# Kernel tuning notes

Hardware: AMD Instinct MI355X
Metric: run time of the kernel (lower is better)

The kernel has to match this reference:

```python
import jax, jax.numpy as jnp
import numpy as np

N, FEAT, PROP, HID, OUT = 8192, 128, 3, 256, 64
IN_SMOOTH = (PROP + 1) * FEAT  # 512
PRELU_INIT = 0.25


def prelu(x, a):
    return jnp.where(x > 0, x, a * x)


def setup_inputs() -> dict:
    key = jax.random.key(0)
    ks = jax.random.split(key, 12)
    s = 0.05
    return {
        "ori_feature": jax.random.normal(ks[0], (N, FEAT), jnp.float32),
        "smoothed_feature": jax.random.normal(ks[1], (N, IN_SMOOTH), jnp.float32),
        "processed_feature": jax.random.normal(ks[2], (N, IN_SMOOTH), jnp.float32),
        "universal_re": jax.random.normal(ks[3], (N, N), jnp.float32),
        # smooth-trans linears
        "Ws1": jax.random.normal(ks[4], (HID, IN_SMOOTH), jnp.float32) * s,
        "bs1": jnp.zeros((HID,), jnp.float32),
        "Ws2": jax.random.normal(ks[5], (OUT, HID), jnp.float32) * s,
        "bs2": jnp.zeros((OUT,), jnp.float32),
        # local-trans linears
        "Wl1": jax.random.normal(ks[6], (HID, FEAT), jnp.float32) * s,
        "bl1": jnp.zeros((HID,), jnp.float32),
        "Wl2": jax.random.normal(ks[7], (OUT, HID), jnp.float32) * s,
        "bl2": jnp.zeros((OUT,), jnp.float32),
        # hete-propagate-layer linears
        "Wh1": jax.random.normal(ks[8], (HID, IN_SMOOTH), jnp.float32) * s,
        "bh1": jnp.zeros((HID,), jnp.float32),
        "Wh2": jax.random.normal(ks[9], (OUT, HID), jnp.float32) * s,
        "bh2": jnp.zeros((OUT,), jnp.float32),
        # PReLU slopes (scalar, one per nn.PReLU())
        "a_model": jnp.float32(PRELU_INIT),
        "a_hete": jnp.float32(PRELU_INIT),
    }


def _getre_scale(emb):
    # emb: [N, OUT]
    es = jax.nn.softmax(emb, axis=1)
    re = es @ es.T                              # [N, N]
    d = jnp.diagonal(re)[:, None]               # [N, 1]
    scaling = d @ d.T                            # [N, N]
    re = re / jnp.maximum(jnp.sqrt(scaling), jnp.float32(1e-9))
    re = re - jnp.diag(jnp.diagonal(re))
    return re


def _forward(ori_feature, smoothed_feature, universal_re,
             Ws1, bs1, Ws2, bs2, Wl1, bl1, Wl2, bl2,
             Wh1, bh1, Wh2, bh2, a_model, a_hete):
    beta = jnp.float32(0.0)  # HetePropagateLayer default beta=0
    # smooth path (dropout is identity in eval)
    h = prelu(smoothed_feature @ Ws1.T + bs1, a_model)
    local_smooth_emb = h @ Ws2.T + bs2
    # local path
    g = prelu(ori_feature @ Wl1.T + bl1, a_model)
    local_ori_emb = g @ Wl2.T + bl2
    # hete propagation on input_prop_feature = smoothed_feature
    f = prelu(smoothed_feature @ Wh1.T + bh1, a_hete)
    feature_emb = f @ Wh2.T + bh2                # [N, OUT]
    re = _getre_scale(feature_emb)               # [N, N]
    lre = beta * universal_re + (1.0 - beta) * re
    m = jnp.mean(lre)
    M = jnp.max(lre)
    pos_diff = M - m                             # pos_min = 0
    shifted = lre - m
    # neg branch: -((shifted - (-m)) / (0 - (-m))) = -((shifted + m) / m)
    lre = jnp.where(shifted > 0, shifted / pos_diff, -((shifted + m) / m))
    # add_diag in source effectively adds identity to its input (bug preserved)
    lre = lre + jnp.eye(N, dtype=lre.dtype)
    pos_signal = prelu(lre, a_hete)
    neg_signal = prelu(-lre, a_hete)
    prop_pos = jax.nn.softmax(pos_signal @ feature_emb, axis=1)
    prop_neg = jax.nn.softmax(neg_signal @ feature_emb, axis=1)
    local_message_propagation = (prop_pos - prop_neg + feature_emb) / 2
    return local_ori_emb, local_smooth_emb, local_message_propagation


def reference(ori_feature, smoothed_feature, processed_feature, universal_re,
              Ws1, bs1, Ws2, bs2, Wl1, bl1, Wl2, bl2,
              Wh1, bh1, Wh2, bh2, a_model, a_hete):
    # processed_feature is unused in the original forward (only .to(device))
    return _forward(ori_feature, smoothed_feature, universal_re,
                    Ws1, bs1, Ws2, bs2, Wl1, bl1, Wl2, bl2,
                    Wh1, bh1, Wh2, bh2, a_model, a_hete)
```

## Files before the change

### kernel.cpp

```cpp
#include <hip/hip_runtime.h>
#include <hip/hip_bf16.h>

#define N 8192

typedef _Float16 half_t;
typedef __attribute__((ext_vector_type(8))) _Float16 half8;
typedef __attribute__((ext_vector_type(4))) float f32x4;
typedef unsigned int uint;
typedef unsigned short ushort;

#define MFMA16(a, b, c) __builtin_amdgcn_mfma_f32_16x16x32_f16(a, b, c, 0, 0, 0)

#define RES_SCALE 2048.0f
#define RES_INV   (1.0f / 2048.0f)

union UH8 { int4 i; half8 h; };
__device__ __forceinline__ half8 ldh(const ushort* p) {
    UH8 t; t.i = *(const int4*)p; return t.h;
}
__device__ __forceinline__ ushort h2u(half_t h) {
    union { half_t f; ushort u; } c; c.f = h; return c.u;
}

__device__ __forceinline__ float wave_max(float v) {
#pragma unroll
    for (int o = 32; o > 0; o >>= 1) v = fmaxf(v, __shfl_xor(v, o, 64));
    return v;
}
__device__ __forceinline__ float wave_sum(float v) {
#pragma unroll
    for (int o = 32; o > 0; o >>= 1) v += __shfl_xor(v, o, 64);
    return v;
}

__global__ __launch_bounds__(256) void gemm_bias_act(
    const float* __restrict__ A, const float* __restrict__ W,
    const float* __restrict__ bias, const float* __restrict__ slope_p,
    float* __restrict__ C, int Nc, int K, int act)
{
    __shared__ float As[16][68];
    __shared__ float Bs[16][68];
    const int tid = threadIdx.x;
    const int tx = tid & 15, ty = tid >> 4;
    const int m0 = blockIdx.x * 64, n0 = blockIdx.y * 64;
    const int lr = tid >> 2, lc4 = (tid & 3) * 4;
    const float* Ap = A + (size_t)(m0 + lr) * K + lc4;
    const float* Wp = W + (size_t)(n0 + lr) * K + lc4;
    float acc[4][4] = {};
    float4 av = *(const float4*)(Ap);
    float4 wv = *(const float4*)(Wp);
    for (int k0 = 0; k0 < K; k0 += 16) {
        __syncthreads();
        As[lc4 + 0][lr] = av.x; As[lc4 + 1][lr] = av.y;
        As[lc4 + 2][lr] = av.z; As[lc4 + 3][lr] = av.w;
        Bs[lc4 + 0][lr] = wv.x; Bs[lc4 + 1][lr] = wv.y;
        Bs[lc4 + 2][lr] = wv.z; Bs[lc4 + 3][lr] = wv.w;
        __syncthreads();
        if (k0 + 16 < K) {
            av = *(const float4*)(Ap + k0 + 16);
            wv = *(const float4*)(Wp + k0 + 16);
        }
#pragma unroll
        for (int k = 0; k < 16; ++k) {
            float a_[4], b_[4];
            float4 t = *(const float4*)&As[k][ty * 4];
            a_[0] = t.x; a_[1] = t.y; a_[2] = t.z; a_[3] = t.w;
            t = *(const float4*)&Bs[k][tx * 4];
            b_[0] = t.x; b_[1] = t.y; b_[2] = t.z; b_[3] = t.w;
#pragma unroll
            for (int i = 0; i < 4; ++i)
#pragma unroll
                for (int j = 0; j < 4; ++j)
                    acc[i][j] += a_[i] * b_[j];
        }
    }
    const float slope = *slope_p;
#pragma unroll
    for (int i = 0; i < 4; ++i) {
        const int row = m0 + ty * 4 + i;
        float4 r;
#pragma unroll
        for (int j = 0; j < 4; ++j) {
            float v = acc[i][j] + bias[n0 + tx * 4 + j];
            if (act) v = v > 0.f ? v : slope * v;
            (&r.x)[j] = v;
        }
        *(float4*)(C + (size_t)row * Nc + n0 + tx * 4) = r;
    }
}

__global__ __launch_bounds__(256) void row_softmax_u(
    const float* __restrict__ E, ushort* __restrict__ uh, ushort* __restrict__ ul,
    float* __restrict__ stats)
{
    const int w = threadIdx.x >> 6, lane = threadIdx.x & 63;
    __shared__ float sacc[4][64];
    __shared__ float tacc[4];
    float s_l = 0.f, t_w = 0.f;
    const int base = blockIdx.x * 16 + w * 4;
    for (int r = 0; r < 4; ++r) {
        const int row = base + r;
        float v = E[(size_t)row * 64 + lane];
        float mx = wave_max(v);
        float e = expf(v - mx);
        float tot = wave_sum(e);
        tot = __shfl(tot, 0, 64);
        float es = e / tot;
        float dd = wave_sum(es * es);
        dd = __shfl(dd, 0, 64);
        float uv = es / sqrtf(dd);
        half_t h = (half_t)uv;
        half_t l = (half_t)((uv - (float)h) * RES_SCALE);
        const size_t idx = (size_t)row * 64 + lane;
        uh[idx] = h2u(h); ul[idx] = h2u(l);
        s_l += uv;
        float uu = wave_sum(uv * uv);
        if (lane == 0) t_w += uu;
    }
    sacc[w][lane] = s_l;
    if (lane == 0) tacc[w] = t_w;
    __syncthreads();
    if (threadIdx.x < 64) {
        float tot = sacc[0][threadIdx.x] + sacc[1][threadIdx.x] +
                    sacc[2][threadIdx.x] + sacc[3][threadIdx.x];
        atomicAdd(&stats[threadIdx.x], tot);
    }
    if (threadIdx.x == 0)
        atomicAdd(&stats[64], tacc[0] + tacc[1] + tacc[2] + tacc[3]);
}

__global__ __launch_bounds__(256) void trans_e(
    const float* __restrict__ E, ushort* __restrict__ Et)
{
    __shared__ ushort T[64][72];
    const int ib = blockIdx.x;
    const int r = threadIdx.x >> 2;
    const int c0 = (threadIdx.x & 3) * 16;
#pragma unroll
    for (int q = 0; q < 4; ++q) {
        float4 v = *(const float4*)(E + (size_t)(ib * 64 + r) * 64 + c0 + q * 4);
#pragma unroll
        for (int t = 0; t < 4; ++t)
            T[c0 + q * 4 + t][r] = h2u((half_t)((&v.x)[t]));
    }
    __syncthreads();
    const int c = threadIdx.x >> 2;
    const int j0 = (threadIdx.x & 3) * 16;
    const size_t go = (size_t)c * N + ib * 64 + j0;
    *(int4*)(Et + go)     = *(const int4*)&T[c][j0];
    *(int4*)(Et + go + 8) = *(const int4*)&T[c][j0 + 8];
}

__global__ __launch_bounds__(64) void pass_max_f16(
    const ushort* __restrict__ uh, const ushort* __restrict__ ul,
    float* __restrict__ maxbuf)
{
    const int bx = blockIdx.x;
    const int by = blockIdx.y;
    const int bid = by * 512 + bx;
    const int i0 = bx * 16;
    const int lane = threadIdx.x;
    const int l16 = lane & 15, lg = lane >> 4;
    if (by * 1024 + 1024 <= i0) {
        if (lane == 0) maxbuf[bid] = 0.f;
        return;
    }
    const size_t ao = (size_t)(i0 + l16) * 64 + lg * 8;
    const half8 Ah0 = ldh(uh + ao), Ah1 = ldh(uh + ao + 32);
    const half8 Al0 = ldh(ul + ao), Al1 = ldh(ul + ao + 32);
    float mx = 0.f;
    for (int jn = 0; jn < 64; ++jn) {
        const int j0 = by * 1024 + jn * 16;
        if (j0 + 16 <= i0) continue;
        const size_t bo = (size_t)(j0 + l16) * 64 + lg * 8;
        half8 Bh0 = ldh(uh + bo), Bh1 = ldh(uh + bo + 32);
        half8 Bl0 = ldh(ul + bo), Bl1 = ldh(ul + bo + 32);
        f32x4 s1 = {0.f, 0.f, 0.f, 0.f};
        f32x4 s2 = {0.f, 0.f, 0.f, 0.f};
        s1 = MFMA16(Ah0, Bh0, s1); s1 = MFMA16(Ah1, Bh1, s1);
        s2 = MFMA16(Ah0, Bl0, s2); s2 = MFMA16(Ah1, Bl1, s2);
        s2 = MFMA16(Al0, Bh0, s2); s2 = MFMA16(Al1, Bh1, s2);
        const bool dt = (j0 == i0);
#pragma unroll
        for (int r = 0; r < 4; ++r) {
            float s = fmaf(s2[r], RES_INV, s1[r]);
            bool dg = dt && (lg * 4 + r == l16);
            mx = dg ? mx : fmaxf(mx, s);
        }
    }
    mx = wave_max(mx);
    if (lane == 0) maxbuf[bid] = mx;
}

__global__ __launch_bounds__(256) void fin_m(
    const float* __restrict__ maxbuf, float* __restrict__ stats)
{
    const int t = threadIdx.x;
    float mx = 0.f;
    for (int i = t; i < 4096; i += 256) mx = fmaxf(mx, maxbuf[i]);
    mx = wave_max(mx);
    __shared__ float red[4];
    __shared__ float ssh;
    if ((t & 63) == 0) red[t >> 6] = mx;
    if (t < 64) {
        float s = stats[t];
        float ss = wave_sum(s * s);
        if (t == 0) ssh = ss;
    }
    __syncthreads();
    if (t == 0) {
        stats[65] = fmaxf(fmaxf(red[0], red[1]), fmaxf(red[2], red[3]));
        stats[66] = (ssh - stats[64]) * (1.0f / 67108864.0f);
    }
}

__global__ __launch_bounds__(256, 4) void pass_prop_f16(
    const ushort* __restrict__ uh, const ushort* __restrict__ ul,
    const ushort* __restrict__ Et, const float* __restrict__ stats,
    const float* __restrict__ ah_p, float* __restrict__ Pp, float* __restrict__ Pn)
{
    __shared__ ushort PNs[4][2][16][68];
    const int w = threadIdx.x >> 6, lane = threadIdx.x & 63;
    const int l16 = lane & 15, lg = lane >> 4;
    const int i0 = blockIdx.x * 16;
    const int js = blockIdx.y;
    const float m = stats[66];
    const float Mx = stats[65];
    const float inv_pd = 1.f / (Mx - m);
    const float c1 = -m * inv_pd;
    const float ninv_m = -1.f / m;
    const float a = *ah_p;
    const size_t ao = (size_t)(i0 + l16) * 64 + lg * 8;
    const half8 Ah0 = ldh(uh + ao), Ah1 = ldh(uh + ao + 32);
    const half8 Al0 = ldh(ul + ao), Al1 = ldh(ul + ao + 32);
    f32x4 accP[4], accN[4];
#pragma unroll
    for (int cs = 0; cs < 4; ++cs) {
        accP[cs] = (f32x4){0.f, 0.f, 0.f, 0.f};
        accN[cs] = (f32x4){0.f, 0.f, 0.f, 0.f};
    }
    ushort (*myP)[68] = PNs[w][0];
    ushort (*myN)[68] = PNs[w][1];
    for (int t = 0; t < 8; ++t) {
        const int j0 = (js * 32 + t * 4 + w) * 64;
#pragma unroll
        for (int jn = 0; jn < 4; ++jn) {
            const size_t bo = (size_t)(j0 + jn * 16 + l16) * 64 + lg * 8;
            half8 Bh0 = ldh(uh + bo), Bh1 = ldh(uh + bo + 32);
            half8 Bl0 = ldh(ul + bo), Bl1 = ldh(ul + bo + 32);
            f32x4 s1 = {0.f, 0.f, 0.f, 0.f};
            f32x4 s2 = {0.f, 0.f, 0.f, 0.f};
            s1 = MFMA16(Ah0, Bh0, s1); s1 = MFMA16(Ah1, Bh1, s1);
            s2 = MFMA16(Ah0, Bl0, s2); s2 = MFMA16(Ah1, Bl1, s2);
            s2 = MFMA16(Al0, Bh0, s2); s2 = MFMA16(Al1, Bh1, s2);
            const bool dt = (j0 + jn * 16 == i0);
#pragma unroll
            for (int r = 0; r < 4; ++r) {
                float s = fmaf(s2[r], RES_INV, s1[r]);
                float l = (s > m) ? fmaf(s, inv_pd, c1) : s * ninv_m;
                if (dt && (lg * 4 + r == l16)) l = 1.0f;
                float q = a * l;
                bool gp = l > 0.f;
                float pos = gp ? l : q;
                float neg = -(gp ? q : l);
                myP[lg * 4 + r][jn * 16 + l16] = h2u((half_t)pos);
                myN[lg * 4 + r][jn * 16 + l16] = h2u((half_t)neg);
            }
        }
#pragma unroll
        for (int kc = 0; kc < 2; ++kc) {
            const ushort* pr = &myP[l16][kc * 32 + lg * 8];
            const ushort* nr = &myN[l16][kc * 32 + lg * 8];
            UH8 tp, tn;
            *(int2*)&tp.i       = *(const int2*)pr;
            *(((int2*)&tp.i)+1) = *(const int2*)(pr + 4);
            *(int2*)&tn.i       = *(const int2*)nr;
            *(((int2*)&tn.i)+1) = *(const int2*)(nr + 4);
            const int ecol = j0 + kc * 32 + lg * 8;
#pragma unroll
            for (int cs = 0; cs < 4; ++cs) {
                const size_t eo = (size_t)(cs * 16 + l16) * N + ecol;
                half8 Ef = ldh(Et + eo);
                accP[cs] = MFMA16(tp.h, Ef, accP[cs]);
                accN[cs] = MFMA16(tn.h, Ef, accN[cs]);
            }
        }
    }
    __syncthreads();
    float* scr = (float*)&PNs[0][0][0][0];
    if (w >= 2) {
        float* base = scr + (size_t)(w - 2) * 2048;
#pragma unroll
        for (int cs = 0; cs < 4; ++cs)
#pragma unroll
            for (int r = 0; r < 4; ++r) {
                const int idx = (lg * 4 + r) * 64 + cs * 16 + l16;
                base[idx]        = accP[cs][r];
                base[idx + 1024] = accN[cs][r];
            }
    }
    __syncthreads();
    if (w < 2) {
        const float* src = scr + (size_t)w * 2048;
#pragma unroll
        for (int cs = 0; cs < 4; ++cs)
#pragma unroll
            for (int r = 0; r < 4; ++r) {
                const int idx = (lg * 4 + r) * 64 + cs * 16 + l16;
                accP[cs][r] += src[idx];
                accN[cs][r] += src[idx + 1024];
            }
    }
    __syncthreads();
    if (w == 1) {
#pragma unroll
        for (int cs = 0; cs < 4; ++cs)
#pragma unroll
            for (int r = 0; r < 4; ++r) {
                const int idx = (lg * 4 + r) * 64 + cs * 16 + l16;
                scr[idx]        = accP[cs][r];
                scr[idx + 1024] = accN[cs][r];
            }
    }
    __syncthreads();
    if (w == 0) {
#pragma unroll
        for (int cs = 0; cs < 4; ++cs)
#pragma unroll
            for (int r = 0; r < 4; ++r) {
                const int idx = (lg * 4 + r) * 64 + cs * 16 + l16;
                const size_t off = ((size_t)js * N + i0 + lg * 4 + r) * 64 + cs * 16 + l16;
                Pp[off] = accP[cs][r] + scr[idx];
                Pn[off] = accN[cs][r] + scr[idx + 1024];
            }
    }
}

__global__ __launch_bounds__(256) void fin_msg(
    const float* __restrict__ Pp, const float* __restrict__ Pn,
    const float* __restrict__ E, float* __restrict__ outm)
{
    const int w = threadIdx.x >> 6, lane = threadIdx.x & 63;
    const int row = blockIdx.x * 4 + w;
    float lp = 0.f, ln = 0.f;
#pragma unroll
    for (int js = 0; js < 4; ++js) {
        lp += Pp[((size_t)js * N + row) * 64 + lane];
        ln += Pn[((size_t)js * N + row) * 64 + lane];
    }
    float mp = wave_max(lp);
    float ep = expf(lp - mp);
    float tp = wave_sum(ep); tp = __shfl(tp, 0, 64);
    float sp = ep / tp;
    float mn = wave_max(ln);
    float en = expf(ln - mn);
    float tn = wave_sum(en); tn = __shfl(tn, 0, 64);
    float sn = en / tn;
    outm[(size_t)row * 64 + lane] = (sp - sn + E[(size_t)row * 64 + lane]) * 0.5f;
}

__global__ void init_stats(float* stats)
{
    if (threadIdx.x < 128) stats[threadIdx.x] = 0.f;
}

extern "C" void kernel_launch(void* const* d_in, const int* in_sizes, int n_in,
                              void* d_out, int out_size, void* d_ws, size_t ws_size,
                              hipStream_t stream)
{
    const float* ori = (const float*)d_in[0];
    const float* smo = (const float*)d_in[1];
    const float* Ws1 = (const float*)d_in[4];
    const float* bs1 = (const float*)d_in[5];
    const float* Ws2 = (const float*)d_in[6];
    const float* bs2 = (const float*)d_in[7];
    const float* Wl1 = (const float*)d_in[8];
    const float* bl1 = (const float*)d_in[9];
    const float* Wl2 = (const float*)d_in[10];
    const float* bl2 = (const float*)d_in[11];
    const float* Wh1 = (const float*)d_in[12];
    const float* bh1 = (const float*)d_in[13];
    const float* Wh2 = (const float*)d_in[14];
    const float* bh2 = (const float*)d_in[15];
    const float* am  = (const float*)d_in[16];
    const float* ah  = (const float*)d_in[17];

    float* out_ori = (float*)d_out;
    float* out_smo = out_ori + (size_t)N * 64;
    float* out_msg = out_smo + (size_t)N * 64;

    char* p = (char*)d_ws;
    float* h      = (float*)p;  p += (size_t)N * 256 * 4;
    float* E      = (float*)p;  p += (size_t)N * 64 * 4;
    float* Pp     = (float*)p;  p += (size_t)4 * N * 64 * 4;
    float* Pn     = (float*)p;  p += (size_t)4 * N * 64 * 4;
    ushort* uh    = (ushort*)p; p += (size_t)N * 64 * 2;
    ushort* ul    = (ushort*)p; p += (size_t)N * 64 * 2;
    ushort* Et    = (ushort*)p; p += (size_t)N * 64 * 2;
    float* maxbuf = (float*)p;  p += 4096 * 4;
    float* stats  = (float*)p;

    const dim3 b(256);
    init_stats<<<1, 128, 0, stream>>>(stats);

    gemm_bias_act<<<dim3(128, 4), b, 0, stream>>>(smo, Ws1, bs1, am, h, 256, 512, 1);
    gemm_bias_act<<<dim3(128, 1), b, 0, stream>>>(h, Ws2, bs2, am, out_smo, 64, 256, 0);
    gemm_bias_act<<<dim3(128, 4), b, 0, stream>>>(ori, Wl1, bl1, am, h, 256, 128, 1);
    gemm_bias_act<<<dim3(128, 1), b, 0, stream>>>(h, Wl2, bl2, am, out_ori, 64, 256, 0);
    gemm_bias_act<<<dim3(128, 4), b, 0, stream>>>(smo, Wh1, bh1, ah, h, 256, 512, 1);
    gemm_bias_act<<<dim3(128, 1), b, 0, stream>>>(h, Wh2, bh2, ah, E, 64, 256, 0);

    row_softmax_u<<<512, b, 0, stream>>>(E, uh, ul, stats);
    trans_e<<<128, b, 0, stream>>>(E, Et);
    pass_max_f16<<<dim3(512, 8), dim3(64), 0, stream>>>(uh, ul, maxbuf);
    fin_m<<<1, 256, 0, stream>>>(maxbuf, stats);
    pass_prop_f16<<<dim3(512, 4), b, 0, stream>>>(uh, ul, Et, stats, ah, Pp, Pn);
    fin_msg<<<2048, b, 0, stream>>>(Pp, Pn, E, out_msg);
}
```

Before: 744.2 us.

## Use split-f16 MFMA GEMMs for linears and regroup max pass into 4-wave blocks

Replaces the scalar FP32 tiled GEMM for the six linear layers with an MFMA kernel that splits inputs and weights into high and low f16 parts and accumulates three products, emulating FP32 accuracy on matrix cores. New split kernels convert inputs and weights each call, and the hidden activations are stored as split f16 pairs. The max pass now runs four waves per block with a shared-memory reduction, which shrinks the partial-max buffer. The prop kernel's launch-bounds occupancy hint is also raised. The trade-off is extra conversion passes and uncoalesced scalar epilogue stores, plus some precision risk from dropping the low-by-low term.

```diff
diff --git a/kernel.cpp b/kernel.cpp
--- a/kernel.cpp
+++ b/kernel.cpp
@@ -33,59 +33,72 @@
     return v;
 }
 
-__global__ __launch_bounds__(256) void gemm_bias_act(
-    const float* __restrict__ A, const float* __restrict__ W,
+__global__ __launch_bounds__(256) void split_f16(
+    const float* __restrict__ X, ushort* __restrict__ Xh, ushort* __restrict__ Xl)
+{
+    const size_t i = ((size_t)blockIdx.x * 256 + threadIdx.x) * 4;
+    float4 v = *(const float4*)(X + i);
+    ushort h[4], l[4];
+#pragma unroll
+    for (int t = 0; t < 4; ++t) {
+        float f = (&v.x)[t];
+        half_t hh = (half_t)f;
+        half_t ll = (half_t)((f - (float)hh) * RES_SCALE);
+        h[t] = h2u(hh); l[t] = h2u(ll);
+    }
+    *(ushort4*)(Xh + i) = make_ushort4(h[0], h[1], h[2], h[3]);
+    *(ushort4*)(Xl + i) = make_ushort4(l[0], l[1], l[2], l[3]);
+}
+
+__global__ __launch_bounds__(128) void gemm_f16s(
+    const ushort* __restrict__ Ah, const ushort* __restrict__ Al,
+    const ushort* __restrict__ Wh, const ushort* __restrict__ Wl,
     const float* __restrict__ bias, const float* __restrict__ slope_p,
-    float* __restrict__ C, int Nc, int K, int act)
-{
-    __shared__ float As[16][68];
-    __shared__ float Bs[16][68];
-    const int tid = threadIdx.x;
-    const int tx = tid & 15, ty = tid >> 4;
-    const int m0 = blockIdx.x * 64, n0 = blockIdx.y * 64;
-    const int lr = tid >> 2, lc4 = (tid & 3) * 4;
-    const float* Ap = A + (size_t)(m0 + lr) * K + lc4;
-    const float* Wp = W + (size_t)(n0 + lr) * K + lc4;
-    float acc[4][4] = {};
-    float4 av = *(const float4*)(Ap);
-    float4 wv = *(const float4*)(Wp);
-    for (int k0 = 0; k0 < K; k0 += 16) {
-        __syncthreads();
-        As[lc4 + 0][lr] = av.x; As[lc4 + 1][lr] = av.y;
-        As[lc4 + 2][lr] = av.z; As[lc4 + 3][lr] = av.w;
-        Bs[lc4 + 0][lr] = wv.x; Bs[lc4 + 1][lr] = wv.y;
-        Bs[lc4 + 2][lr] = wv.z; Bs[lc4 + 3][lr] = wv.w;
-        __syncthreads();
-        if (k0 + 16 < K) {
-            av = *(const float4*)(Ap + k0 + 16);
-            wv = *(const float4*)(Wp + k0 + 16);
+    int Nc, int K, int act,
+    float* __restrict__ Cf, ushort* __restrict__ Ch, ushort* __restrict__ Cl)
+{
+    const int w = threadIdx.x >> 6, lane = threadIdx.x & 63;
+    const int l16 = lane & 15, lg = lane >> 4;
+    const int row0 = blockIdx.x * 32 + w * 16;
+    const int n0 = blockIdx.y * 64;
+    f32x4 acc1[4], acc2[4];
+#pragma unroll
+    for (int c = 0; c < 4; ++c) {
+        acc1[c] = (f32x4){0.f, 0.f, 0.f, 0.f};
+        acc2[c] = (f32x4){0.f, 0.f, 0.f, 0.f};
+    }
+    for (int k0 = 0; k0 < K; k0 += 32) {
+        const size_t aoff = (size_t)(row0 + l16) * K + lg * 8 + k0;
+        half8 Af = ldh(Ah + aoff);
+        half8 Alf = ldh(Al + aoff);
+#pragma unroll
+        for (int c = 0; c < 4; ++c) {
+            const size_t woff = (size_t)(n0 + c * 16 + l16) * K + lg * 8 + k0;
+            half8 Wf = ldh(Wh + woff);
+            half8 Wlf = ldh(Wl + woff);
+            acc1[c] = MFMA16(Af, Wf, acc1[c]);
+            acc2[c] = MFMA16(Af, Wlf, acc2[c]);
+            acc2[c] = MFMA16(Alf, Wf, acc2[c]);
         }
-#pragma unroll
-        for (int k = 0; k < 16; ++k) {
-            float a_[4], b_[4];
-            float4 t = *(const float4*)&As[k][ty * 4];
-            a_[0] = t.x; a_[1] = t.y; a_[2] = t.z; a_[3] = t.w;
-            t = *(const float4*)&Bs[k][tx * 4];
-            b_[0] = t.x; b_[1] = t.y; b_[2] = t.z; b_[3] = t.w;
-#pragma unroll
-            for (int i = 0; i < 4; ++i)
-#pragma unroll
-                for (int j = 0; j < 4; ++j)
-                    acc[i][j] += a_[i] * b_[j];
+    }
+    const float slope = *slope_p;
+#pragma unroll
+    for (int c = 0; c < 4; ++c) {
+        const int col = n0 + c * 16 + l16;
+        const float b = bias[col];
+#pragma unroll
+        for (int r = 0; r < 4; ++r) {
+            const int row = row0 + lg * 4 + r;
+            float v = fmaf(acc2[c][r], RES_INV, acc1[c][r]) + b;
+            if (act) v = v > 0.f ? v : slope * v;
+            const size_t off = (size_t)row * Nc + col;
+            if (Cf) Cf[off] = v;
+            if (Ch) {
+                half_t hh = (half_t)v;
+                half_t ll = (half_t)((v - (float)hh) * RES_SCALE);
+                Ch[off] = h2u(hh); Cl[off] = h2u(ll);
+            }
         }
-    }
-    const float slope = *slope_p;
-#pragma unroll
-    for (int i = 0; i < 4; ++i) {
-        const int row = m0 + ty * 4 + i;
-        float4 r;
-#pragma unroll
-        for (int j = 0; j < 4; ++j) {
-            float v = acc[i][j] + bias[n0 + tx * 4 + j];
-            if (act) v = v > 0.f ? v : slope * v;
-            (&r.x)[j] = v;
-        }
-        *(float4*)(C + (size_t)row * Nc + n0 + tx * 4) = r;
     }
 }
 
@@ -151,20 +164,21 @@
     *(int4*)(Et + go + 8) = *(const int4*)&T[c][j0 + 8];
 }
 
-__global__ __launch_bounds__(64) void pass_max_f16(
+__global__ __launch_bounds__(256) void pass_max_f16(
     const ushort* __restrict__ uh, const ushort* __restrict__ ul,
     float* __restrict__ maxbuf)
 {
     const int bx = blockIdx.x;
     const int by = blockIdx.y;
-    const int bid = by * 512 + bx;
-    const int i0 = bx * 16;
-    const int lane = threadIdx.x;
+    const int bid = by * 128 + bx;
+    const int w = threadIdx.x >> 6, lane = threadIdx.x & 63;
     const int l16 = lane & 15, lg = lane >> 4;
-    if (by * 1024 + 1024 <= i0) {
-        if (lane == 0) maxbuf[bid] = 0.f;
+    __shared__ float red[4];
+    if (by * 1024 + 1024 <= bx * 64) {
+        if (threadIdx.x == 0) maxbuf[bid] = 0.f;
         return;
     }
+    const int i0 = bx * 64 + w * 16;
     const size_t ao = (size_t)(i0 + l16) * 64 + lg * 8;
     const half8 Ah0 = ldh(uh + ao), Ah1 = ldh(uh + ao + 32);
     const half8 Al0 = ldh(ul + ao), Al1 = ldh(ul + ao + 32);
@@ -189,7 +203,10 @@
         }
     }
     mx = wave_max(mx);
-    if (lane == 0) maxbuf[bid] = mx;
+    if (lane == 0) red[w] = mx;
+    __syncthreads();
+    if (threadIdx.x == 0)
+        maxbuf[bid] = fmaxf(fmaxf(red[0], red[1]), fmaxf(red[2], red[3]));
 }
 
 __global__ __launch_bounds__(256) void fin_m(
@@ -197,7 +214,7 @@
 {
     const int t = threadIdx.x;
     float mx = 0.f;
-    for (int i = t; i < 4096; i += 256) mx = fmaxf(mx, maxbuf[i]);
+    for (int i = t; i < 1024; i += 256) mx = fmaxf(mx, maxbuf[i]);
     mx = wave_max(mx);
     __shared__ float red[4];
     __shared__ float ssh;
@@ -214,7 +231,7 @@
     }
 }
 
-__global__ __launch_bounds__(256, 4) void pass_prop_f16(
+__global__ __launch_bounds__(256, 8) void pass_prop_f16(
     const ushort* __restrict__ uh, const ushort* __restrict__ ul,
     const ushort* __restrict__ Et, const float* __restrict__ stats,
     const float* __restrict__ ah_p, float* __restrict__ Pp, float* __restrict__ Pn)
@@ -390,29 +407,62 @@
     float* out_msg = out_smo + (size_t)N * 64;
 
     char* p = (char*)d_ws;
-    float* h      = (float*)p;  p += (size_t)N * 256 * 4;
+    ushort* hh    = (ushort*)p; p += (size_t)N * 256 * 2;
+    ushort* hl    = (ushort*)p; p += (size_t)N * 256 * 2;
     float* E      = (float*)p;  p += (size_t)N * 64 * 4;
     float* Pp     = (float*)p;  p += (size_t)4 * N * 64 * 4;
     float* Pn     = (float*)p;  p += (size_t)4 * N * 64 * 4;
     ushort* uh    = (ushort*)p; p += (size_t)N * 64 * 2;
     ushort* ul    = (ushort*)p; p += (size_t)N * 64 * 2;
     ushort* Et    = (ushort*)p; p += (size_t)N * 64 * 2;
-    float* maxbuf = (float*)p;  p += 4096 * 4;
+    ushort* orih  = (ushort*)p; p += (size_t)N * 128 * 2;
+    ushort* oril  = (ushort*)p; p += (size_t)N * 128 * 2;
+    ushort* Ws1h  = (ushort*)p; p += 256 * 512 * 2;
+    ushort* Ws1l  = (ushort*)p; p += 256 * 512 * 2;
+    ushort* Ws2h  = (ushort*)p; p += 64 * 256 * 2;
+    ushort* Ws2l  = (ushort*)p; p += 64 * 256 * 2;
+    ushort* Wl1h  = (ushort*)p; p += 256 * 128 * 2;
+    ushort* Wl1l  = (ushort*)p; p += 256 * 128 * 2;
+    ushort* Wl2h  = (ushort*)p; p += 64 * 256 * 2;
+    ushort* Wl2l  = (ushort*)p; p += 64 * 256 * 2;
+    ushort* Wh1h  = (ushort*)p; p += 256 * 512 * 2;
+    ushort* Wh1l  = (ushort*)p; p += 256 * 512 * 2;
+    ushort* Wh2h  = (ushort*)p; p += 64 * 256 * 2;
+    ushort* Wh2l  = (ushort*)p; p += 64 * 256 * 2;
+    float* maxbuf = (float*)p;  p += 1024 * 4;
     float* stats  = (float*)p;
+    ushort* smoh = (ushort*)Pp;
+    ushort* smol = (ushort*)Pn;
 
     const dim3 b(256);
     init_stats<<<1, 128, 0, stream>>>(stats);
 
-    gemm_bias_act<<<dim3(128, 4), b, 0, stream>>>(smo, Ws1, bs1, am, h, 256, 512, 1);
-    gemm_bias_act<<<dim3(128, 1), b, 0, stream>>>(h, Ws2, bs2, am, out_smo, 64, 256, 0);
-    gemm_bias_act<<<dim3(128, 4), b, 0, stream>>>(ori, Wl1, bl1, am, h, 256, 128, 1);
-    gemm_bias_act<<<dim3(128, 1), b, 0, stream>>>(h, Wl2, bl2, am, out_ori, 64, 256, 0);
-    gemm_bias_act<<<dim3(128, 4), b, 0, stream>>>(smo, Wh1, bh1, ah, h, 256, 512, 1);
-    gemm_bias_act<<<dim3(128, 1), b, 0, stream>>>(h, Wh2, bh2, ah, E, 64, 256, 0);
+    split_f16<<<4096, b, 0, stream>>>(smo, smoh, smol);
+    split_f16<<<1024, b, 0, stream>>>(ori, orih, oril);
+    split_f16<<<128,  b, 0, stream>>>(Ws1, Ws1h, Ws1l);
+    split_f16<<<16,   b, 0, stream>>>(Ws2, Ws2h, Ws2l);
+    split_f16<<<32,   b, 0, stream>>>(Wl1, Wl1h, Wl1l);
+    split_f16<<<16,   b, 0, stream>>>(Wl2, Wl2h, Wl2l);
+    split_f16<<<128,  b, 0, stream>>>(Wh1, Wh1h, Wh1l);
+    split_f16<<<16,   b, 0, stream>>>(Wh2, Wh2h, Wh2l);
+
+    const dim3 gb(128);
+    gemm_f16s<<<dim3(256, 4), gb, 0, stream>>>(smoh, smol, Ws1h, Ws1l, bs1, am,
+                                               256, 512, 1, nullptr, hh, hl);
+    gemm_f16s<<<dim3(256, 1), gb, 0, stream>>>(hh, hl, Ws2h, Ws2l, bs2, am,
+                                               64, 256, 0, out_smo, nullptr, nullptr);
+    gemm_f16s<<<dim3(256, 4), gb, 0, stream>>>(orih, oril, Wl1h, Wl1l, bl1, am,
+                                               256, 128, 1, nullptr, hh, hl);
+    gemm_f16s<<<dim3(256, 1), gb, 0, stream>>>(hh, hl, Wl2h, Wl2l, bl2, am,
+                                               64, 256, 0, out_ori, nullptr, nullptr);
+    gemm_f16s<<<dim3(256, 4), gb, 0, stream>>>(smoh, smol, Wh1h, Wh1l, bh1, ah,
+                                               256, 512, 1, nullptr, hh, hl);
+    gemm_f16s<<<dim3(256, 1), gb, 0, stream>>>(hh, hl, Wh2h, Wh2l, bh2, ah,
+                                               64, 256, 0, E, nullptr, nullptr);
 
     row_softmax_u<<<512, b, 0, stream>>>(E, uh, ul, stats);
     trans_e<<<128, b, 0, stream>>>(E, Et);
-    pass_max_f16<<<dim3(512, 8), dim3(64), 0, stream>>>(uh, ul, maxbuf);
+    pass_max_f16<<<dim3(128, 8), b, 0, stream>>>(uh, ul, maxbuf);
     fin_m<<<1, 256, 0, stream>>>(maxbuf, stats);
     pass_prop_f16<<<dim3(512, 4), b, 0, stream>>>(uh, ul, Et, stats, ah, Pp, Pn);
     fin_msg<<<2048, b, 0, stream>>>(Pp, Pn, E, out_msg);
```

New measurement: 880.0 us. 1.18x slower.
